# Optimization experiments

Measured on AMD Instinct MI355X. Metric: run time of the kernel, lower is better.

Reference implementation:

```python
import jax, jax.numpy as jnp
import numpy as np

N_EMBD = 1024
N_HEAD = 16
HEAD_DIM = N_EMBD // N_HEAD


def setup_inputs() -> dict:
    key = jax.random.key(0)
    ks = jax.random.split(key, 9)
    B, T, C = 2, 2048, N_EMBD
    s = 1.0 / np.sqrt(C)
    inp = {
        "x": jax.random.normal(ks[0], (B, T, C), dtype=jnp.float32),
        "Wq": jax.random.normal(ks[1], (C, C), dtype=jnp.float32) * s,
        "bq": jnp.zeros((C,), dtype=jnp.float32),
        "Wk": jax.random.normal(ks[2], (C, C), dtype=jnp.float32) * s,
        "bk": jnp.zeros((C,), dtype=jnp.float32),
        "Wv": jax.random.normal(ks[3], (C, C), dtype=jnp.float32) * s,
        "bv": jnp.zeros((C,), dtype=jnp.float32),
        "Wo": jax.random.normal(ks[4], (C, C), dtype=jnp.float32) * s,
        "bo": jnp.zeros((C,), dtype=jnp.float32),
    }
    return inp


def reference(x, Wq, bq, Wk, bk, Wv, bv, Wo, bo):
    B, T, C = x.shape
    H, D = N_HEAD, HEAD_DIM
    # projections (torch Linear: x @ W^T + b)
    q = (x @ Wq.T + bq).reshape(B, T, H, D).transpose(0, 2, 1, 3)  # [B,H,T,D]
    k = (x @ Wk.T + bk).reshape(B, T, H, D).transpose(0, 2, 1, 3)
    v = (x @ Wv.T + bv).reshape(B, T, H, D).transpose(0, 2, 1, 3)
    scores = jnp.einsum("bhqd,bhkd->bhqk", q, k) / jnp.sqrt(jnp.asarray(D, x.dtype))
    causal = jnp.tril(jnp.ones((T, T), dtype=bool))
    scores = jnp.where(causal[None, None], scores, jnp.asarray(-jnp.inf, x.dtype))
    weights = jax.nn.softmax(scores, axis=-1)  # [B,H,T,T]
    attended = jnp.einsum("bhqk,bhkd->bhqd", weights, v)
    attended = attended.transpose(0, 2, 1, 3).reshape(B, T, C)
    return attended @ Wo.T + bo
```

## Files before the change

### kernel.cpp

```cpp
#include <hip/hip_runtime.h>

typedef unsigned short u16;
typedef __attribute__((ext_vector_type(8))) __bf16 bf16x8;
typedef __attribute__((ext_vector_type(4))) float f32x4;
typedef __attribute__((ext_vector_type(4))) unsigned int u32x4;

#define MFMA16(a, b, c) __builtin_amdgcn_mfma_f32_16x16x32_bf16(a, b, c, 0, 0, 0)

__device__ __forceinline__ u16 f2bf(float f) {
    unsigned u = __float_as_uint(f);
    u = (u + 0x7FFFu + ((u >> 16) & 1u)) >> 16;
    return (u16)u;
}

__device__ __forceinline__ void gl_lds16(const u16* g, u16* l) {
    __builtin_amdgcn_global_load_lds(
        (const __attribute__((address_space(1))) unsigned int*)g,
        (__attribute__((address_space(3))) unsigned int*)l, 16, 0, 0);
}

static constexpr int Bv = 2, Tv = 2048, Cv = 1024, Hv = 16, Dv = 64;
static constexpr int Mv = Bv * Tv;

static constexpr size_t OFF_XB = 0;
static constexpr size_t OFF_WQ = 4194304;
static constexpr size_t OFF_WK = OFF_WQ + 1048576;
static constexpr size_t OFF_WV = OFF_WK + 1048576;
static constexpr size_t OFF_WO = OFF_WV + 1048576;
static constexpr size_t OFF_Q  = OFF_WO + 1048576;
static constexpr size_t OFF_K  = OFF_Q + 4194304;
static constexpr size_t OFF_VT = OFF_K + 4194304;
static constexpr size_t OFF_A  = OFF_VT + 4194304;

__global__ __launch_bounds__(256) void convert_all(
    const float* __restrict__ x,
    const float* __restrict__ wq, const float* __restrict__ wk,
    const float* __restrict__ wv, const float* __restrict__ wo,
    u16* __restrict__ dst)
{
    int i4 = blockIdx.x * blockDim.x + threadIdx.x;
    if (i4 >= 2097152) return;
    int idx = i4 * 4;
    const float* src; int off;
    if (idx < 4194304) { src = x; off = idx; }
    else {
        int rel = idx - 4194304;
        int j = rel >> 20;
        off = rel & 1048575;
        src = (j == 0) ? wq : (j == 1) ? wk : (j == 2) ? wv : wo;
    }
    float4 v = *(const float4*)(src + off);
    ushort4 o;
    o.x = f2bf(v.x); o.y = f2bf(v.y); o.z = f2bf(v.z); o.w = f2bf(v.w);
    *(ushort4*)(dst + idx) = o;
}

template <bool OUT_BF16, bool ROWBIAS>
__device__ __forceinline__ void gemm128_b32(
    u16* __restrict__ lA0, u16* __restrict__ lB0,
    u16* __restrict__ lA1, u16* __restrict__ lB1,
    const u16* __restrict__ A, const u16* __restrict__ Wt,
    const float* __restrict__ bias, void* __restrict__ outp,
    int m0, int n0, int N, int K)
{
    const int tid  = threadIdx.x;
    const int lane = tid & 63, w = tid >> 6;
    const int quad = lane >> 4, lm = lane & 15;
    const int wm = (w & 1) * 64, wn = (w >> 1) * 64;
    const int h4A = (w & 1) * 4, h4B = ((w >> 1) & 1) * 4;
    const int rowi = lane >> 3, seg = lane & 7;
    const int raw = seg ^ rowi;
    const int hh  = raw >> 2, qq = raw & 3;

    f32x4 zero = {0.f, 0.f, 0.f, 0.f};
    f32x4 acc[4][4];
    #pragma unroll
    for (int mt = 0; mt < 4; mt++)
        #pragma unroll
        for (int nt = 0; nt < 4; nt++) acc[mt][nt] = zero;

    auto stage = [&](u16* dA, u16* dB, int k0) __attribute__((always_inline)) {
        #pragma unroll
        for (int j = 0; j < 2; j++) {
            int pr0 = w * 16 + j * 8;
            int gr  = pr0 + rowi + (hh << 6);
            gl_lds16(A  + (size_t)(m0 + gr) * K + k0 + qq * 8, &dA[pr0 * 64]);
            gl_lds16(Wt + (size_t)(n0 + gr) * K + k0 + qq * 8, &dB[pr0 * 64]);
        }
    };
    auto compute = [&](const u16* sA, const u16* sB) __attribute__((always_inline)) {
        bf16x8 af[4], bf[4];
        #pragma unroll
        for (int mt = 0; mt < 4; mt++)
            af[mt] = *(const bf16x8*)&sA[(mt * 16 + lm) * 64 + (((h4A + quad) ^ (lm & 7)) * 8)];
        #pragma unroll
        for (int nt = 0; nt < 4; nt++)
            bf[nt] = *(const bf16x8*)&sB[(nt * 16 + lm) * 64 + (((h4B + quad) ^ (lm & 7)) * 8)];
        #pragma unroll
        for (int mt = 0; mt < 4; mt++)
            #pragma unroll
            for (int nt = 0; nt < 4; nt++)
                acc[mt][nt] = MFMA16(af[mt], bf[nt], acc[mt][nt]);
    };

    const int NT = K >> 5;
    stage(lA0, lB0, 0);
    stage(lA1, lB1, 32);
    for (int t = 0; t < NT; ++t) {
        if (t + 1 < NT) asm volatile("s_waitcnt vmcnt(4)" ::: "memory");
        else            asm volatile("s_waitcnt vmcnt(0)" ::: "memory");
        __builtin_amdgcn_s_barrier();
        const u16* sA = (t & 1) ? lA1 : lA0;
        const u16* sB = (t & 1) ? lB1 : lB0;
        compute(sA, sB);
        asm volatile("s_waitcnt lgkmcnt(0)" ::: "memory");
        __builtin_amdgcn_s_barrier();
        if (t + 2 < NT) stage((t & 1) ? lA1 : lA0, (t & 1) ? lB1 : lB0, (t + 2) << 5);
    }

    #pragma unroll
    for (int nt = 0; nt < 4; nt++) {
        int col = n0 + wn + nt * 16 + lm;
        float cb = ROWBIAS ? 0.f : bias[col];
        #pragma unroll
        for (int mt = 0; mt < 4; mt++) {
            #pragma unroll
            for (int r = 0; r < 4; r++) {
                int row = m0 + wm + mt * 16 + quad * 4 + r;
                float v = acc[mt][nt][r] + (ROWBIAS ? bias[row] : cb);
                if (OUT_BF16) ((u16*)outp)[(size_t)row * N + col] = f2bf(v);
                else          ((float*)outp)[(size_t)row * N + col] = v;
            }
        }
    }
}

__global__ __launch_bounds__(256, 3) void gemm_qkv(
    const u16* __restrict__ A,
    const u16* __restrict__ Wq, const u16* __restrict__ Wk, const u16* __restrict__ Wv,
    const float* __restrict__ bq, const float* __restrict__ bk, const float* __restrict__ bv,
    u16* __restrict__ Q, u16* __restrict__ K, u16* __restrict__ VT)
{
    __shared__ u16 lA0[64 * 64];
    __shared__ u16 lB0[64 * 64];
    __shared__ u16 lA1[64 * 64];
    __shared__ u16 lB1[64 * 64];

    int bid = blockIdx.x;
    int sw  = (bid & 7) * 96 + (bid >> 3);
    int g2  = sw >> 5;
    int row = sw & 31;
    int which = g2 >> 3, col = g2 & 7;

    if (which == 0) {
        gemm128_b32<true, false>(lA0, lB0, lA1, lB1, A, Wq, bq, Q, row * 128, col * 128, Cv, Cv);
    } else if (which == 1) {
        gemm128_b32<true, false>(lA0, lB0, lA1, lB1, A, Wk, bk, K, row * 128, col * 128, Cv, Cv);
    } else {
        gemm128_b32<true, true>(lA0, lB0, lA1, lB1, Wv, A, bv, VT, col * 128, row * 128, Mv, Cv);
    }
}

__global__ __launch_bounds__(512) void gemm_o64(
    const u16* __restrict__ A, const u16* __restrict__ Wt,
    const float* __restrict__ bias, float* __restrict__ outp)
{
    __shared__ u16 lA0[128 * 64];
    __shared__ u16 lA1[128 * 64];
    __shared__ u16 lB0[64 * 64];
    __shared__ u16 lB1[64 * 64];

    const int tid  = threadIdx.x;
    const int lane = tid & 63, w = tid >> 6;
    const int quad = lane >> 4, lm = lane & 15;
    const int wm = (w & 3) * 32, wn = (w >> 2) * 32;

    int bid = blockIdx.x;
    int sw  = (bid & 7) * 64 + (bid >> 3);
    const int n0 = (sw >> 5) * 64;
    const int m0 = (sw & 31) * 128;
    const int K = Cv;
    const int rowi = lane >> 3, seg = lane & 7;

    f32x4 zero = {0.f, 0.f, 0.f, 0.f};
    f32x4 acc[2][2];
    #pragma unroll
    for (int mt = 0; mt < 2; mt++)
        #pragma unroll
        for (int nt = 0; nt < 2; nt++) acc[mt][nt] = zero;

    auto stage = [&](u16* dA, u16* dB, int k0) __attribute__((always_inline)) {
        #pragma unroll
        for (int i = 0; i < 2; i++) {
            int rbase = w * 16 + i * 8;
            int row = rbase + rowi;
            int gseg = seg ^ (row & 7);
            gl_lds16(A + (size_t)(m0 + row) * K + k0 + gseg * 8, &dA[rbase * 64]);
        }
        {
            int rbase = w * 8, row = rbase + rowi;
            gl_lds16(Wt + (size_t)(n0 + row) * K + k0 + ((seg ^ (row & 7))) * 8, &dB[rbase * 64]);
        }
    };
    auto compute = [&](const u16* sA, const u16* sB) __attribute__((always_inline)) {
        #pragma unroll
        for (int ks = 0; ks < 2; ks++) {
            const int swz = ((ks * 4 + quad) ^ (lm & 7)) * 8;
            bf16x8 af[2], bf[2];
            #pragma unroll
            for (int mt = 0; mt < 2; mt++)
                af[mt] = *(const bf16x8*)&sA[(wm + mt * 16 + lm) * 64 + swz];
            #pragma unroll
            for (int nt = 0; nt < 2; nt++)
                bf[nt] = *(const bf16x8*)&sB[(wn + nt * 16 + lm) * 64 + swz];
            #pragma unroll
            for (int mt = 0; mt < 2; mt++)
                #pragma unroll
                for (int nt = 0; nt < 2; nt++)
                    acc[mt][nt] = MFMA16(af[mt], bf[nt], acc[mt][nt]);
        }
    };

    const int NT = K >> 6;
    stage(lA0, lB0, 0);
    stage(lA1, lB1, 64);
    for (int t = 0; t < NT; ++t) {
        if (t + 1 < NT) asm volatile("s_waitcnt vmcnt(3)" ::: "memory");
        else            asm volatile("s_waitcnt vmcnt(0)" ::: "memory");
        __builtin_amdgcn_s_barrier();
        u16* sA = (t & 1) ? lA1 : lA0;
        u16* sB = (t & 1) ? lB1 : lB0;
        compute(sA, sB);
        asm volatile("s_waitcnt lgkmcnt(0)" ::: "memory");
        __builtin_amdgcn_s_barrier();
        if (t + 2 < NT) stage(sA, sB, (t + 2) << 6);
    }

    #pragma unroll
    for (int nt = 0; nt < 2; nt++) {
        int col = n0 + wn + nt * 16 + lm;
        float bvv = bias[col];
        #pragma unroll
        for (int mt = 0; mt < 2; mt++) {
            #pragma unroll
            for (int r = 0; r < 4; r++) {
                int row = m0 + wm + mt * 16 + quad * 4 + r;
                outp[(size_t)row * Cv + col] = acc[mt][nt][r] + bvv;
            }
        }
    }
}

__global__ __launch_bounds__(512) void attn(
    const u16* __restrict__ Qp, const u16* __restrict__ Kp,
    const u16* __restrict__ VTg, u16* __restrict__ Op)
{
    __shared__ u16 lK[2][64 * 64];
    __shared__ u16 lVT[2][64 * 64];
    __shared__ u16 lP[8][32][72];

    const int tid  = threadIdx.x;
    const int lane = tid & 63, w = tid >> 6;
    const int g = w >> 2, wl = w & 3;
    const int quad = lane >> 4, lm = lane & 15;

    const int idx  = blockIdx.x;
    const int half = idx >> 8;
    const int grp  = idx & 255;
    const int bh   = (half << 4) | (grp >> 4);
    const int j    = grp & 15;
    const int qt   = half ? j : 15 - j;
    const int h = bh & 15, b = bh >> 4;

    const int qb = qt * 128;
    const size_t headoff = (size_t)b * Tv * Cv + (size_t)h * Dv;
    const size_t vthead  = (size_t)h * 64 * Mv + (size_t)b * Tv;

    bf16x8 qf[2][2];
    #pragma unroll
    for (int nt = 0; nt < 2; nt++) {
        const u16* qptr = Qp + headoff + (size_t)(qb + wl * 32 + nt * 16 + lm) * Cv + quad * 8;
        qf[0][nt] = *(const bf16x8*)(qptr);
        qf[1][nt] = *(const bf16x8*)(qptr + 32);
    }

    f32x4 zero = {0.f, 0.f, 0.f, 0.f};
    f32x4 oacc[2][4];
    #pragma unroll
    for (int mt = 0; mt < 2; mt++)
        #pragma unroll
        for (int nt = 0; nt < 4; nt++) oacc[mt][nt] = zero;
    float Lp[2] = {0.f, 0.f};

    const float SC = 0.18033688011112042f;
    const int rowi = lane >> 3, seg = lane & 7;

    auto stage = [&](int kt) {
        const int k0 = kt * 64;
        #pragma unroll
        for (int hf = 0; hf < 2; hf++) {
            int rbase = wl * 16 + hf * 8;
            int row = rbase + rowi;
            int gseg = seg ^ (row & 7);
            gl_lds16(Kp + headoff + (size_t)(k0 + row) * Cv + gseg * 8, &lK[g][rbase * 64]);
            gl_lds16(VTg + vthead + (size_t)row * Mv + k0 + gseg * 8, &lVT[g][rbase * 64]);
        }
    };

    auto body = [&](int kt, bool domask) __attribute__((always_inline)) {
        const int k0 = kt * 64;
        f32x4 stt[4][2];
        #pragma unroll
        for (int mt = 0; mt < 4; mt++)
            #pragma unroll
            for (int nt = 0; nt < 2; nt++) stt[mt][nt] = zero;
        #pragma unroll
        for (int ks = 0; ks < 2; ks++) {
            #pragma unroll
            for (int mt = 0; mt < 4; mt++) {
                bf16x8 kf = *(const bf16x8*)
                    &lK[g][(mt * 16 + lm) * 64 + (((ks * 4 + quad) ^ (lm & 7)) * 8)];
                #pragma unroll
                for (int nt = 0; nt < 2; nt++)
                    stt[mt][nt] = MFMA16(kf, qf[ks][nt], stt[mt][nt]);
            }
        }
        #pragma unroll
        for (int mt = 0; mt < 4; mt++) {
            #pragma unroll
            for (int nt = 0; nt < 2; nt++) {
                const int keyb = k0 + mt * 16 + quad * 4;
                const int qrow = qb + wl * 32 + nt * 16 + lm;
                float e0 = __builtin_amdgcn_exp2f(fmaf(stt[mt][nt][0], SC, -16.f));
                float e1 = __builtin_amdgcn_exp2f(fmaf(stt[mt][nt][1], SC, -16.f));
                float e2 = __builtin_amdgcn_exp2f(fmaf(stt[mt][nt][2], SC, -16.f));
                float e3 = __builtin_amdgcn_exp2f(fmaf(stt[mt][nt][3], SC, -16.f));
                if (domask) {
                    if (keyb + 0 > qrow) e0 = 0.f;
                    if (keyb + 1 > qrow) e1 = 0.f;
                    if (keyb + 2 > qrow) e2 = 0.f;
                    if (keyb + 3 > qrow) e3 = 0.f;
                }
                Lp[nt] += e0 + e1 + e2 + e3;
                ushort4 pk;
                pk.x = (u16)(__float_as_uint(e0) >> 16);
                pk.y = (u16)(__float_as_uint(e1) >> 16);
                pk.z = (u16)(__float_as_uint(e2) >> 16);
                pk.w = (u16)(__float_as_uint(e3) >> 16);
                *(ushort4*)&lP[w][nt * 16 + lm][mt * 16 + quad * 4] = pk;
            }
        }
        #pragma unroll
        for (int ks = 0; ks < 2; ks++) {
            bf16x8 pf[2];
            #pragma unroll
            for (int mt = 0; mt < 2; mt++)
                pf[mt] = *(const bf16x8*)&lP[w][mt * 16 + lm][ks * 32 + quad * 8];
            #pragma unroll
            for (int nt = 0; nt < 4; nt++) {
                bf16x8 vf = *(const bf16x8*)
                    &lVT[g][(nt * 16 + lm) * 64 + (((ks * 4 + quad) ^ (lm & 7)) * 8)];
                #pragma unroll
                for (int mt = 0; mt < 2; mt++)
                    oacc[mt][nt] = MFMA16(pf[mt], vf, oacc[mt][nt]);
            }
        }
    };

    for (int i = 0; i < qt; i++) {
        if (i) __syncthreads();
        stage(2 * i + g);
        __syncthreads();
        body(2 * i + g, false);
    }
    if (qt) __syncthreads();
    stage(2 * qt + g);
    __syncthreads();
    body(2 * qt + g, true);
    __syncthreads();

    float* lO = (float*)&lP[0][0][0];
    float* lL = lO + 32 * 256;
    const int t = tid & 255;
    if (g == 1) {
        #pragma unroll
        for (int mt = 0; mt < 2; mt++)
            #pragma unroll
            for (int nt = 0; nt < 4; nt++)
                #pragma unroll
                for (int r = 0; r < 4; r++)
                    lO[(mt * 16 + nt * 4 + r) * 256 + t] = oacc[mt][nt][r];
        lL[t] = Lp[0];
        lL[256 + t] = Lp[1];
    }
    __syncthreads();
    if (g == 0) {
        #pragma unroll
        for (int mt = 0; mt < 2; mt++)
            #pragma unroll
            for (int nt = 0; nt < 4; nt++)
                #pragma unroll
                for (int r = 0; r < 4; r++)
                    oacc[mt][nt][r] += lO[(mt * 16 + nt * 4 + r) * 256 + t];
        Lp[0] += lL[t];
        Lp[1] += lL[256 + t];

        float Lred[2];
        #pragma unroll
        for (int nt = 0; nt < 2; nt++) {
            float L = Lp[nt];
            L += __shfl_xor(L, 16, 64);
            L += __shfl_xor(L, 32, 64);
            Lred[nt] = 1.0f / L;
        }
        #pragma unroll
        for (int mt = 0; mt < 2; mt++) {
            float inv[4];
            #pragma unroll
            for (int r = 0; r < 4; r++)
                inv[r] = __shfl(Lred[mt], (lane & 48) | (quad * 4 + r), 64);
            #pragma unroll
            for (int nt = 0; nt < 4; nt++) {
                #pragma unroll
                for (int r = 0; r < 4; r++) {
                    int row = qb + wl * 32 + mt * 16 + quad * 4 + r;
                    Op[headoff + (size_t)row * Cv + nt * 16 + lm] = f2bf(oacc[mt][nt][r] * inv[r]);
                }
            }
        }
    }
}

extern "C" void kernel_launch(void* const* d_in, const int* in_sizes, int n_in,
                              void* d_out, int out_size, void* d_ws, size_t ws_size,
                              hipStream_t stream) {
    const float* x  = (const float*)d_in[0];
    const float* Wq = (const float*)d_in[1];
    const float* bq = (const float*)d_in[2];
    const float* Wk = (const float*)d_in[3];
    const float* bk = (const float*)d_in[4];
    const float* Wv = (const float*)d_in[5];
    const float* bv = (const float*)d_in[6];
    const float* Wo = (const float*)d_in[7];
    const float* bo = (const float*)d_in[8];
    u16* ws = (u16*)d_ws;

    convert_all<<<8192, 256, 0, stream>>>(x, Wq, Wk, Wv, Wo, ws);

    gemm_qkv<<<768, 256, 0, stream>>>(
        ws + OFF_XB, ws + OFF_WQ, ws + OFF_WK, ws + OFF_WV,
        bq, bk, bv, ws + OFF_Q, ws + OFF_K, ws + OFF_VT);

    attn<<<512, 512, 0, stream>>>(ws + OFF_Q, ws + OFF_K, ws + OFF_VT, ws + OFF_A);

    gemm_o64<<<512, 512, 0, stream>>>(ws + OFF_A, ws + OFF_WO, bo, (float*)d_out);
}
```

Baseline: 177.1 us.

## Prefetch next K/V tile into registers during attention body

Replaces direct global-to-LDS loads with a register-staged software pipeline: the next K and V^T tiles are loaded into registers in the middle of the current tile's compute, then written to LDS at the start of the next iteration. This is meant to hide global load latency behind the softmax and PV MFMA work instead of stalling after each stage. It also raises wave priority around the MFMA sections with s_setprio. The cost is extra VGPRs, which could lower occupancy, plus explicit LDS stores in place of async LDS loads.

```diff
diff --git a/kernel.cpp b/kernel.cpp
--- a/kernel.cpp
+++ b/kernel.cpp
@@ -295,25 +295,34 @@
     const float SC = 0.18033688011112042f;
     const int rowi = lane >> 3, seg = lane & 7;
 
-    auto stage = [&](int kt) {
+    u32x4 rK[2], rV[2];
+    auto ldregs = [&](int kt) __attribute__((always_inline)) {
         const int k0 = kt * 64;
+        #pragma unroll
+        for (int hf = 0; hf < 2; hf++) {
+            int row = wl * 16 + hf * 8 + rowi;
+            int gseg = seg ^ (row & 7);
+            rK[hf] = *(const u32x4*)(Kp + headoff + (size_t)(k0 + row) * Cv + gseg * 8);
+            rV[hf] = *(const u32x4*)(VTg + vthead + (size_t)row * Mv + k0 + gseg * 8);
+        }
+    };
+    auto wrregs = [&]() __attribute__((always_inline)) {
         #pragma unroll
         for (int hf = 0; hf < 2; hf++) {
             int rbase = wl * 16 + hf * 8;
-            int row = rbase + rowi;
-            int gseg = seg ^ (row & 7);
-            gl_lds16(Kp + headoff + (size_t)(k0 + row) * Cv + gseg * 8, &lK[g][rbase * 64]);
-            gl_lds16(VTg + vthead + (size_t)row * Mv + k0 + gseg * 8, &lVT[g][rbase * 64]);
-        }
-    };
-
-    auto body = [&](int kt, bool domask) __attribute__((always_inline)) {
+            *(u32x4*)&lK[g][rbase * 64 + lane * 8] = rK[hf];
+            *(u32x4*)&lVT[g][rbase * 64 + lane * 8] = rV[hf];
+        }
+    };
+
+    auto body = [&](int kt, bool domask, bool prefetch, int nextkt) __attribute__((always_inline)) {
         const int k0 = kt * 64;
         f32x4 stt[4][2];
         #pragma unroll
         for (int mt = 0; mt < 4; mt++)
             #pragma unroll
             for (int nt = 0; nt < 2; nt++) stt[mt][nt] = zero;
+        __builtin_amdgcn_s_setprio(1);
         #pragma unroll
         for (int ks = 0; ks < 2; ks++) {
             #pragma unroll
@@ -325,6 +334,7 @@
                     stt[mt][nt] = MFMA16(kf, qf[ks][nt], stt[mt][nt]);
             }
         }
+        __builtin_amdgcn_s_setprio(0);
         #pragma unroll
         for (int mt = 0; mt < 4; mt++) {
             #pragma unroll
@@ -350,6 +360,8 @@
                 *(ushort4*)&lP[w][nt * 16 + lm][mt * 16 + quad * 4] = pk;
             }
         }
+        if (prefetch) ldregs(nextkt);
+        __builtin_amdgcn_s_setprio(1);
         #pragma unroll
         for (int ks = 0; ks < 2; ks++) {
             bf16x8 pf[2];
@@ -365,18 +377,16 @@
                     oacc[mt][nt] = MFMA16(pf[mt], vf, oacc[mt][nt]);
             }
         }
-    };
-
-    for (int i = 0; i < qt; i++) {
+        __builtin_amdgcn_s_setprio(0);
+    };
+
+    ldregs(g);
+    for (int i = 0; i <= qt; i++) {
         if (i) __syncthreads();
-        stage(2 * i + g);
+        wrregs();
         __syncthreads();
-        body(2 * i + g, false);
-    }
-    if (qt) __syncthreads();
-    stage(2 * qt + g);
-    __syncthreads();
-    body(2 * qt + g, true);
+        body(2 * i + g, i == qt, i < qt, 2 * (i + 1) + g);
+    }
     __syncthreads();
 
     float* lO = (float*)&lP[0][0][0];
```

Result: no change. 180.6 us (+2.0%).

## Restructure attention into 4-wave blocks with double-buffered K/V prefetch pipeline

Applied to the files above, without the earlier changes.

The attention kernel previously split each query tile's keys across two 4-wave groups that worked on alternate key tiles and merged their partial outputs through shared memory at the end. Now one 4-wave block walks all key tiles sequentially. It prefetches two tiles ahead into a double buffer and waits on explicit vmcnt counts, so loads overlap compute. MFMA phases are also raised with s_setprio. This removes the cross-group reduction and halves LDS for P, but halves the threads per block, which may reduce latency hiding.

```diff
diff --git a/kernel.cpp b/kernel.cpp
--- a/kernel.cpp
+++ b/kernel.cpp
@@ -251,17 +251,16 @@
     }
 }
 
-__global__ __launch_bounds__(512) void attn(
+__global__ __launch_bounds__(256) void attn(
     const u16* __restrict__ Qp, const u16* __restrict__ Kp,
     const u16* __restrict__ VTg, u16* __restrict__ Op)
 {
     __shared__ u16 lK[2][64 * 64];
     __shared__ u16 lVT[2][64 * 64];
-    __shared__ u16 lP[8][32][72];
+    __shared__ u16 lP[4][32][72];
 
     const int tid  = threadIdx.x;
     const int lane = tid & 63, w = tid >> 6;
-    const int g = w >> 2, wl = w & 3;
     const int quad = lane >> 4, lm = lane & 15;
 
     const int idx  = blockIdx.x;
@@ -279,7 +278,7 @@
     bf16x8 qf[2][2];
     #pragma unroll
     for (int nt = 0; nt < 2; nt++) {
-        const u16* qptr = Qp + headoff + (size_t)(qb + wl * 32 + nt * 16 + lm) * Cv + quad * 8;
+        const u16* qptr = Qp + headoff + (size_t)(qb + w * 32 + nt * 16 + lm) * Cv + quad * 8;
         qf[0][nt] = *(const bf16x8*)(qptr);
         qf[1][nt] = *(const bf16x8*)(qptr + 32);
     }
@@ -295,42 +294,44 @@
     const float SC = 0.18033688011112042f;
     const int rowi = lane >> 3, seg = lane & 7;
 
-    auto stage = [&](int kt) {
+    auto stage = [&](int buf, int kt) __attribute__((always_inline)) {
         const int k0 = kt * 64;
         #pragma unroll
         for (int hf = 0; hf < 2; hf++) {
-            int rbase = wl * 16 + hf * 8;
+            int rbase = w * 16 + hf * 8;
             int row = rbase + rowi;
             int gseg = seg ^ (row & 7);
-            gl_lds16(Kp + headoff + (size_t)(k0 + row) * Cv + gseg * 8, &lK[g][rbase * 64]);
-            gl_lds16(VTg + vthead + (size_t)row * Mv + k0 + gseg * 8, &lVT[g][rbase * 64]);
-        }
-    };
-
-    auto body = [&](int kt, bool domask) __attribute__((always_inline)) {
+            gl_lds16(Kp + headoff + (size_t)(k0 + row) * Cv + gseg * 8, &lK[buf][rbase * 64]);
+            gl_lds16(VTg + vthead + (size_t)row * Mv + k0 + gseg * 8, &lVT[buf][rbase * 64]);
+        }
+    };
+
+    auto body = [&](int buf, int kt, bool domask) __attribute__((always_inline)) {
         const int k0 = kt * 64;
         f32x4 stt[4][2];
         #pragma unroll
         for (int mt = 0; mt < 4; mt++)
             #pragma unroll
             for (int nt = 0; nt < 2; nt++) stt[mt][nt] = zero;
+        __builtin_amdgcn_s_setprio(1);
         #pragma unroll
         for (int ks = 0; ks < 2; ks++) {
             #pragma unroll
             for (int mt = 0; mt < 4; mt++) {
                 bf16x8 kf = *(const bf16x8*)
-                    &lK[g][(mt * 16 + lm) * 64 + (((ks * 4 + quad) ^ (lm & 7)) * 8)];
+                    &lK[buf][(mt * 16 + lm) * 64 + (((ks * 4 + quad) ^ (lm & 7)) * 8)];
                 #pragma unroll
                 for (int nt = 0; nt < 2; nt++)
                     stt[mt][nt] = MFMA16(kf, qf[ks][nt], stt[mt][nt]);
             }
         }
+        __builtin_amdgcn_s_setprio(0);
         #pragma unroll
         for (int mt = 0; mt < 4; mt++) {
             #pragma unroll
             for (int nt = 0; nt < 2; nt++) {
                 const int keyb = k0 + mt * 16 + quad * 4;
-                const int qrow = qb + wl * 32 + nt * 16 + lm;
+                const int qrow = qb + w * 32 + nt * 16 + lm;
                 float e0 = __builtin_amdgcn_exp2f(fmaf(stt[mt][nt][0], SC, -16.f));
                 float e1 = __builtin_amdgcn_exp2f(fmaf(stt[mt][nt][1], SC, -16.f));
                 float e2 = __builtin_amdgcn_exp2f(fmaf(stt[mt][nt][2], SC, -16.f));
@@ -350,6 +351,7 @@
                 *(ushort4*)&lP[w][nt * 16 + lm][mt * 16 + quad * 4] = pk;
             }
         }
+        __builtin_amdgcn_s_setprio(1);
         #pragma unroll
         for (int ks = 0; ks < 2; ks++) {
             bf16x8 pf[2];
@@ -359,73 +361,48 @@
             #pragma unroll
             for (int nt = 0; nt < 4; nt++) {
                 bf16x8 vf = *(const bf16x8*)
-                    &lVT[g][(nt * 16 + lm) * 64 + (((ks * 4 + quad) ^ (lm & 7)) * 8)];
+                    &lVT[buf][(nt * 16 + lm) * 64 + (((ks * 4 + quad) ^ (lm & 7)) * 8)];
                 #pragma unroll
                 for (int mt = 0; mt < 2; mt++)
                     oacc[mt][nt] = MFMA16(pf[mt], vf, oacc[mt][nt]);
             }
         }
-    };
-
-    for (int i = 0; i < qt; i++) {
-        if (i) __syncthreads();
-        stage(2 * i + g);
-        __syncthreads();
-        body(2 * i + g, false);
-    }
-    if (qt) __syncthreads();
-    stage(2 * qt + g);
-    __syncthreads();
-    body(2 * qt + g, true);
-    __syncthreads();
-
-    float* lO = (float*)&lP[0][0][0];
-    float* lL = lO + 32 * 256;
-    const int t = tid & 255;
-    if (g == 1) {
-        #pragma unroll
-        for (int mt = 0; mt < 2; mt++)
-            #pragma unroll
-            for (int nt = 0; nt < 4; nt++)
-                #pragma unroll
-                for (int r = 0; r < 4; r++)
-                    lO[(mt * 16 + nt * 4 + r) * 256 + t] = oacc[mt][nt][r];
-        lL[t] = Lp[0];
-        lL[256 + t] = Lp[1];
-    }
-    __syncthreads();
-    if (g == 0) {
-        #pragma unroll
-        for (int mt = 0; mt < 2; mt++)
-            #pragma unroll
-            for (int nt = 0; nt < 4; nt++)
-                #pragma unroll
-                for (int r = 0; r < 4; r++)
-                    oacc[mt][nt][r] += lO[(mt * 16 + nt * 4 + r) * 256 + t];
-        Lp[0] += lL[t];
-        Lp[1] += lL[256 + t];
-
-        float Lred[2];
-        #pragma unroll
-        for (int nt = 0; nt < 2; nt++) {
-            float L = Lp[nt];
-            L += __shfl_xor(L, 16, 64);
-            L += __shfl_xor(L, 32, 64);
-            Lred[nt] = 1.0f / L;
-        }
-        #pragma unroll
-        for (int mt = 0; mt < 2; mt++) {
-            float inv[4];
-            #pragma unroll
-            for (int r = 0; r < 4; r++)
-                inv[r] = __shfl(Lred[mt], (lane & 48) | (quad * 4 + r), 64);
-            #pragma unroll
-            for (int nt = 0; nt < 4; nt++) {
-                #pragma unroll
-                for (int r = 0; r < 4; r++) {
-                    int row = qb + wl * 32 + mt * 16 + quad * 4 + r;
-                    Op[headoff + (size_t)row * Cv + nt * 16 + lm] = f2bf(oacc[mt][nt][r] * inv[r]);
-                }
+        __builtin_amdgcn_s_setprio(0);
+    };
+
+    const int NT = 2 * qt + 2;
+    stage(0, 0);
+    stage(1, 1);
+    for (int i = 0; i < NT; i++) {
+        if (i + 1 < NT) asm volatile("s_waitcnt vmcnt(4)" ::: "memory");
+        else            asm volatile("s_waitcnt vmcnt(0)" ::: "memory");
+        __builtin_amdgcn_s_barrier();
+        body(i & 1, i, i >= 2 * qt);
+        asm volatile("s_waitcnt lgkmcnt(0)" ::: "memory");
+        __builtin_amdgcn_s_barrier();
+        if (i + 2 < NT) stage(i & 1, i + 2);
+    }
+
+    float Lred[2];
+    #pragma unroll
+    for (int nt = 0; nt < 2; nt++) {
+        float L = Lp[nt];
+        L += __shfl_xor(L, 16, 64);
+        L += __shfl_xor(L, 32, 64);
+        Lred[nt] = 1.0f / L;
+    }
+    #pragma unroll
+    for (int mt = 0; mt < 2; mt++) {
+        float inv[4];
+        #pragma unroll
+        for (int r = 0; r < 4; r++)
+            inv[r] = __shfl(Lred[mt], (lane & 48) | (quad * 4 + r), 64);
+        #pragma unroll
+        for (int nt = 0; nt < 4; nt++) {
+            #pragma unroll
+            for (int r = 0; r < 4; r++) {
+                int row = qb + w * 32 + mt * 16 + quad * 4 + r;
+                Op[headoff + (size_t)row * Cv + nt * 16 + lm] = f2bf(oacc[mt][nt][r] * inv[r]);
             }
         }
     }
@@ -451,7 +428,7 @@
         ws + OFF_XB, ws + OFF_WQ, ws + OFF_WK, ws + OFF_WV,
         bq, bk, bv, ws + OFF_Q, ws + OFF_K, ws + OFF_VT);
 
-    attn<<<512, 512, 0, stream>>>(ws + OFF_Q, ws + OFF_K, ws + OFF_VT, ws + OFF_A);
+    attn<<<512, 256, 0, stream>>>(ws + OFF_Q, ws + OFF_K, ws + OFF_VT, ws + OFF_A);
 
     gemm_o64<<<512, 512, 0, stream>>>(ws + OFF_A, ws + OFF_WO, bo, (float*)d_out);
 }
```

Result: slower. 189.0 us (+6.7%).
